# Optimization experiments

Hardware: AMD Instinct MI355X
Metric: run time of the kernel (lower is better)

Reference implementation:

```python
import jax, jax.numpy as jnp
import numpy as np

B, T = 32, 2048            # batch, seq_len
V = 16                     # vocab_size
H = 256                    # hidden_size
NV = V + 2                 # embedding rows (padding_idx=0 + vocab + delimiter)
NO = V + 1                 # head output size


def setup_inputs() -> dict:
    key = jax.random.key(0)
    ks = jax.random.split(key, 8)
    s = 1.0 / np.sqrt(H).astype(np.float32)
    tokens = jax.random.randint(ks[0], (B, T), 0, NV)
    embed = jax.random.normal(ks[1], (NV, H), jnp.float32) * 0.02
    embed = embed.at[0].set(0.0)  # padding_idx=0
    # GRU params (PyTorch layout: gates [r|z|n] stacked on last dim)
    W_ih = jax.random.uniform(ks[2], (H, 3 * H), jnp.float32, -s, s)
    W_hh = jax.random.uniform(ks[3], (H, 3 * H), jnp.float32, -s, s)
    b_ih = jax.random.uniform(ks[4], (3 * H,), jnp.float32, -s, s)
    b_hh = jax.random.uniform(ks[5], (3 * H,), jnp.float32, -s, s)
    W_head = jax.random.uniform(ks[6], (H, NO), jnp.float32, -s, s)
    b_head = jax.random.uniform(ks[7], (NO,), jnp.float32, -s, s)
    return {"tokens": tokens, "embed": embed, "W_ih": W_ih, "W_hh": W_hh,
            "b_ih": b_ih, "b_hh": b_hh, "W_head": W_head, "b_head": b_head}


def _mogru_scan(x, W_ih, W_hh, b_ih, b_hh):
    # x: [B, T, H]. Precompute all input projections in one big GEMM.
    gi = x @ W_ih + b_ih                      # [B, T, 3H]
    gi_t = jnp.swapaxes(gi, 0, 1)             # [T, B, 3H] for scan
    h0 = jnp.zeros((x.shape[0], W_hh.shape[0]), x.dtype)

    def step(h, gi_step):
        gh = h @ W_hh + b_hh                  # [B, 3H]
        i_r, i_z, i_n = jnp.split(gi_step, 3, axis=-1)
        h_r, h_z, h_n = jnp.split(gh, 3, axis=-1)
        r = jax.nn.sigmoid(i_r + h_r)
        z = jax.nn.sigmoid(i_z + h_z)         # beta: retention gate
        n = jnp.tanh(i_n + r * h_n)
        h_new = (1.0 - z) * n + z * h
        return h_new, (h_new, z)

    h_last, (outs, betas) = jax.lax.scan(step, h0, gi_t)
    return jnp.swapaxes(outs, 0, 1), h_last, jnp.swapaxes(betas, 0, 1)


def reference(tokens, embed, W_ih, W_hh, b_ih, b_hh, W_head, b_head):
    x = embed[tokens]                          # [B, T, H] embedding lookup
    output, _, betas = _mogru_scan(x, W_ih, W_hh, b_ih, b_hh)
    logits = output @ W_head + b_head          # [B, T, V+1]
    return logits, betas
```

## Files before the change

### kernel.cpp

```cpp
#include <hip/hip_runtime.h>

#define BB   32
#define TT   2048
#define HH   256
#define G3   768
#define NVOC 18
#define NOUT 17
#define LOGITS_ELEMS ((size_t)BB * TT * NOUT)

typedef _Float16 h2 __attribute__((ext_vector_type(2)));

__device__ __forceinline__ float bf1(unsigned short u){
  union{unsigned int i; float f;} v; v.i = ((unsigned int)u) << 16; return v.f;
}
__device__ __forceinline__ unsigned short f2bf(float f){
  union{float f; unsigned int i;} v; v.f = f;
  unsigned int lsb = (v.i >> 16) & 1u;
  v.i += 0x7fffu + lsb;
  return (unsigned short)(v.i >> 16);
}
__device__ __forceinline__ float bflo(unsigned int u){
  union{unsigned int i; float f;} v; v.i = u << 16; return v.f;
}
__device__ __forceinline__ float bfhi(unsigned int u){
  union{unsigned int i; float f;} v; v.i = u & 0xffff0000u; return v.f;
}

__device__ __forceinline__ float ld1(const float* p, size_t i){ return p[i]; }
__device__ __forceinline__ float ld1(const unsigned short* p, size_t i){ return bf1(p[i]); }

__device__ __forceinline__ bool detect_f32(const void* W_ih_raw){
  const unsigned short* u = (const unsigned short*)W_ih_raw;
  bool big = false;
  #pragma unroll
  for (int i = 0; i < 64; i++){
    float v = bf1(u[i]);
    big |= !(v >= -0.25f && v <= 0.25f);
  }
  return big;
}

#if __has_builtin(__builtin_amdgcn_fdot2)
#define FDOT2(a,b,c) __builtin_amdgcn_fdot2((a),(b),(c),false)
#else
#define FDOT2(a,b,c) ((c) + (float)(a).x*(float)(b).x + (float)(a).y*(float)(b).y)
#endif

template<typename T>
__device__ __forceinline__ void prep_body(const T* W_hh, _Float16* Wp){
  int j = blockIdx.x;
  int e = threadIdx.x;
  int q = j & 1, p = j >> 1;
  int c = e >> 7, i = e & 127;
  float v = ld1(W_hh, (size_t)(128*q + i) * G3 + 2*p + c);
  Wp[(size_t)j * 256 + e] = (_Float16)v;
}

__global__ __launch_bounds__(256) void k_prep(
    const void* __restrict__ W_hh, const void* __restrict__ W_ih,
    _Float16* __restrict__ Wp)
{
  if (detect_f32(W_ih)) prep_body<float>((const float*)W_hh, Wp);
  else                  prep_body<unsigned short>((const unsigned short*)W_hh, Wp);
}

template<typename T>
__device__ __forceinline__ void proj_body(const T* embed, const T* W_ih,
                                          const T* b_ih, const T* b_hh,
                                          float* proj, float* bb){
  __shared__ float s_e[HH];
  int v = blockIdx.x, j = threadIdx.x;
  if (j < HH) s_e[j] = ld1(embed, (size_t)v * HH + j);
  if (v == 0) bb[j] = ld1(b_hh, (size_t)j);
  __syncthreads();
  float acc = ld1(b_ih, (size_t)j);
  #pragma unroll 8
  for (int k = 0; k < HH; k++)
    acc += s_e[k] * ld1(W_ih, (size_t)k * G3 + j);
  proj[(size_t)v * G3 + j] = acc;
}

__global__ __launch_bounds__(768) void k_proj(
    const void* __restrict__ embed, const void* __restrict__ W_ih,
    const void* __restrict__ b_ih, const void* __restrict__ b_hh,
    float* __restrict__ proj, float* __restrict__ bb)
{
  if (detect_f32(W_ih))
    proj_body<float>((const float*)embed, (const float*)W_ih,
                     (const float*)b_ih, (const float*)b_hh, proj, bb);
  else
    proj_body<unsigned short>((const unsigned short*)embed,
                              (const unsigned short*)W_ih,
                              (const unsigned short*)b_ih,
                              (const unsigned short*)b_hh, proj, bb);
}

__global__ __launch_bounds__(768, 1) void k_scan(
    const int*      __restrict__ tokens,
    const _Float16* __restrict__ Wp,
    const float*    __restrict__ bb,
    const void*     __restrict__ W_ih,
    const float*    __restrict__ proj,
    unsigned short* __restrict__ outs,
    void*           __restrict__ d_out_base)
{
  __shared__ float s_proj[NVOC * G3];
  __shared__ __align__(16) h2 s_h[HH / 2];
  __shared__ float s_z[HH];
  __shared__ float s_n[HH];

  const bool f32m = detect_f32(W_ih);
  const int b = blockIdx.x;
  const int j = threadIdx.x;
  const int q16 = (j & 1) * 16;

  for (int i = j; i < NVOC * G3; i += 768) s_proj[i] = proj[i];

  h2 wA[64], wB[64];
  {
    const float4* wp4 = (const float4*)(Wp + (size_t)j * 256);
    #pragma unroll
    for (int i = 0; i < 16; i++){
      float4 v = wp4[i];
      wA[4*i+0] = __builtin_bit_cast(h2, v.x);
      wA[4*i+1] = __builtin_bit_cast(h2, v.y);
      wA[4*i+2] = __builtin_bit_cast(h2, v.z);
      wA[4*i+3] = __builtin_bit_cast(h2, v.w);
    }
    #pragma unroll
    for (int i = 0; i < 16; i++){
      float4 v = wp4[16 + i];
      wB[4*i+0] = __builtin_bit_cast(h2, v.x);
      wB[4*i+1] = __builtin_bit_cast(h2, v.y);
      wB[4*i+2] = __builtin_bit_cast(h2, v.z);
      wB[4*i+3] = __builtin_bit_cast(h2, v.w);
    }
  }
  const float bhh = bb[j];

  if (j < HH/2) { h2 z; z.x = (_Float16)0.f; z.y = (_Float16)0.f; s_h[j] = z; }
  float h_old = 0.f;

  const int* tptr = tokens + (size_t)b * TT;
  int tok = tptr[0];
  unsigned short* orow   = outs + (size_t)b * TT * HH + j;
  unsigned short* brow_b = (unsigned short*)d_out_base + LOGITS_ELEMS
                           + (size_t)b * TT * HH + (j - HH);
  float*          brow_f = (float*)d_out_base + LOGITS_ELEMS
                           + (size_t)b * TT * HH + (j - HH);

  __syncthreads();

  for (int t = 0; t < TT; t++) {
    int tok_next = (t + 1 < TT) ? tptr[t + 1] : 0;
    const float* pj = s_proj + tok * G3;
    float gi  = pj[j];
    float gin = (j < HH) ? pj[2*HH + j] : 0.f;

    float a0 = 0.f, a1 = 0.f, a2 = 0.f, a3 = 0.f;
    const int4* hp = (const int4*)s_h;
    #pragma unroll
    for (int i = 0; i < 16; i++) {
      int4 hv = hp[q16 + i];
      h2 x0 = __builtin_bit_cast(h2, hv.x);
      h2 x1 = __builtin_bit_cast(h2, hv.y);
      h2 x2 = __builtin_bit_cast(h2, hv.z);
      h2 x3 = __builtin_bit_cast(h2, hv.w);
      a0 = FDOT2(wA[4*i+0], x0, a0);
      a1 = FDOT2(wA[4*i+1], x1, a1);
      a0 = FDOT2(wA[4*i+2], x2, a0);
      a1 = FDOT2(wA[4*i+3], x3, a1);
      a2 = FDOT2(wB[4*i+0], x0, a2);
      a3 = FDOT2(wB[4*i+1], x1, a3);
      a2 = FDOT2(wB[4*i+2], x2, a2);
      a3 = FDOT2(wB[4*i+3], x3, a3);
    }
    float accA = a0 + a1;
    float accB = a2 + a3;
    accA += __shfl_xor(accA, 1);
    accB += __shfl_xor(accB, 1);
    float gh = ((j & 1) ? accB : accA) + bhh;

    float r = 0.f;
    if (j >= 2*HH) {
      s_n[j - 2*HH] = gh;
    } else if (j >= HH) {
      float z = 1.f / (1.f + __expf(-(gi + gh)));
      s_z[j - HH] = z;
      if (f32m) brow_f[(size_t)t * HH] = z;
      else      brow_b[(size_t)t * HH] = f2bf(z);
    } else {
      r = 1.f / (1.f + __expf(-(gi + gh)));
    }
    __syncthreads();

    if (j < HH) {
      float z = s_z[j];
      float x = gin + r * s_n[j];
      x = fminf(fmaxf(x, -15.f), 15.f);
      float e = __expf(2.f * x);
      float n = (e - 1.f) / (e + 1.f);
      float hn = (1.f - z) * n + z * h_old;
      h_old = hn;
      ((_Float16*)s_h)[j] = (_Float16)hn;
      orow[(size_t)t * HH] = f2bf(hn);
    }
    __syncthreads();
    tok = tok_next;
  }
}

template<typename T>
__device__ __forceinline__ void stage_head(const T* W_head, const T* b_head,
                                           float* s_w, float* s_b, int tid){
  for (int i = tid; i < NOUT * HH; i += 256) {
    int o = i / HH, k = i - o * HH;
    s_w[i] = ld1(W_head, (size_t)k * NOUT + o);
  }
  if (tid < NOUT) s_b[tid] = ld1(b_head, (size_t)tid);
}

__global__ __launch_bounds__(256) void k_head(
    const unsigned short* __restrict__ outs,
    const void* __restrict__ W_head,
    const void* __restrict__ b_head,
    const void* __restrict__ W_ih,
    void* __restrict__ logits_out)
{
  __shared__ float s_w[NOUT * HH];
  __shared__ float s_b[NOUT];
  const bool f32m = detect_f32(W_ih);
  const int tid = threadIdx.x;

  if (f32m) stage_head<float>((const float*)W_head, (const float*)b_head,
                              s_w, s_b, tid);
  else      stage_head<unsigned short>((const unsigned short*)W_head,
                                       (const unsigned short*)b_head,
                                       s_w, s_b, tid);
  __syncthreads();

  size_t gid = (size_t)blockIdx.x * 256 + tid;
  if (gid >= LOGITS_ELEMS) return;
  int o = (int)(gid % NOUT);
  size_t row = gid / NOUT;

  const uint4* xp = (const uint4*)(outs + row * HH);
  const float* wv = s_w + o * HH;
  float a0 = 0.f, a1 = 0.f, a2 = 0.f, a3 = 0.f;
  #pragma unroll 8
  for (int kk = 0; kk < 32; kk++) {
    uint4 u = xp[kk];
    int kb = kk * 8;
    a0 += bflo(u.x) * wv[kb+0] + bfhi(u.x) * wv[kb+1];
    a1 += bflo(u.y) * wv[kb+2] + bfhi(u.y) * wv[kb+3];
    a2 += bflo(u.z) * wv[kb+4] + bfhi(u.z) * wv[kb+5];
    a3 += bflo(u.w) * wv[kb+6] + bfhi(u.w) * wv[kb+7];
  }
  float val = ((a0 + a1) + (a2 + a3)) + s_b[o];
  if (f32m) ((float*)logits_out)[gid] = val;
  else      ((unsigned short*)logits_out)[gid] = f2bf(val);
}

extern "C" void kernel_launch(void* const* d_in, const int* in_sizes, int n_in,
                              void* d_out, int out_size, void* d_ws, size_t ws_size,
                              hipStream_t stream)
{
  const int* tokens = (const int*)d_in[0];
  const void* embed  = d_in[1];
  const void* W_ih   = d_in[2];
  const void* W_hh   = d_in[3];
  const void* b_ih   = d_in[4];
  const void* b_hh   = d_in[5];
  const void* W_head = d_in[6];
  const void* b_head = d_in[7];

  char* ws = (char*)d_ws;
  float*          proj = (float*)ws;
  float*          bb   = (float*)(ws + 55296);
  _Float16*       Wp   = (_Float16*)(ws + 55296 + 3072);
  unsigned short* outs = (unsigned short*)(ws + 55296 + 3072 + 393216);

  k_prep<<<G3, 256, 0, stream>>>(W_hh, W_ih, Wp);
  k_proj<<<NVOC, G3, 0, stream>>>(embed, W_ih, b_ih, b_hh, proj, bb);
  k_scan<<<BB, G3, 0, stream>>>(tokens, Wp, bb, W_ih, proj, outs, d_out);
  k_head<<<(int)((LOGITS_ELEMS + 255) / 256), 256, 0, stream>>>(
      outs, W_head, b_head, W_ih, d_out);
}
```

Before: 2.718 ms.

## Restructure GRU scan to 512 threads with all three gates per pair and double-buffered h

The scan kernel now uses 512 threads, where each thread pair owns one hidden unit and computes its r, z and n gate dot products from 192 register-resident fp16 weight pairs. The gate combine runs in registers instead of through shared memory. Double-buffering the hidden state cuts the per-step barriers from two to one. The r/z parts of b_hh are folded into the precomputed input projection, the weight prep layout is rewritten to match, and the h buffers are padded to avoid bank conflicts. The cost is much higher register pressure (192 h2 weights per thread), which could cause spills.

Result: slower. 2.786 ms (+2.5%).

```diff
diff --git a/kernel.cpp b/kernel.cpp
--- a/kernel.cpp
+++ b/kernel.cpp
@@ -47,18 +47,24 @@
 #endif
 
 template<typename T>
-__device__ __forceinline__ void prep_body(const T* W_hh, _Float16* Wp){
-  int j = blockIdx.x;
-  int e = threadIdx.x;
-  int q = j & 1, p = j >> 1;
-  int c = e >> 7, i = e & 127;
-  float v = ld1(W_hh, (size_t)(128*q + i) * G3 + 2*p + c);
-  Wp[(size_t)j * 256 + e] = (_Float16)v;
+__device__ __forceinline__ void prep_body(const T* W_hh, unsigned int* Wp){
+  unsigned int e = blockIdx.x * 256 + threadIdx.x;
+  unsigned int c = e & 3, tmp = e >> 2;
+  unsigned int tid = tmp & 511, f = tmp >> 9;
+  unsigned int m = (f << 2) | c;
+  unsigned int g = m >> 6, kk = m & 63;
+  unsigned int u = tid >> 1, q = tid & 1;
+  unsigned int col = g * 256 + u;
+  unsigned int k0 = q * 128 + kk * 2;
+  float lo = ld1(W_hh, (size_t)k0 * G3 + col);
+  float hi = ld1(W_hh, (size_t)(k0 + 1) * G3 + col);
+  h2 t; t.x = (_Float16)lo; t.y = (_Float16)hi;
+  Wp[e] = __builtin_bit_cast(unsigned int, t);
 }
 
 __global__ __launch_bounds__(256) void k_prep(
     const void* __restrict__ W_hh, const void* __restrict__ W_ih,
-    _Float16* __restrict__ Wp)
+    unsigned int* __restrict__ Wp)
 {
   if (detect_f32(W_ih)) prep_body<float>((const float*)W_hh, Wp);
   else                  prep_body<unsigned short>((const unsigned short*)W_hh, Wp);
@@ -74,6 +80,7 @@
   if (v == 0) bb[j] = ld1(b_hh, (size_t)j);
   __syncthreads();
   float acc = ld1(b_ih, (size_t)j);
+  if (j < 2 * HH) acc += ld1(b_hh, (size_t)j);
   #pragma unroll 8
   for (int k = 0; k < HH; k++)
     acc += s_e[k] * ld1(W_ih, (size_t)k * G3 + j);
@@ -95,119 +102,115 @@
                               (const unsigned short*)b_hh, proj, bb);
 }
 
-__global__ __launch_bounds__(768, 1) void k_scan(
-    const int*      __restrict__ tokens,
-    const _Float16* __restrict__ Wp,
-    const float*    __restrict__ bb,
-    const void*     __restrict__ W_ih,
-    const float*    __restrict__ proj,
-    unsigned short* __restrict__ outs,
-    void*           __restrict__ d_out_base)
-{
-  __shared__ float s_proj[NVOC * G3];
-  __shared__ __align__(16) h2 s_h[HH / 2];
-  __shared__ float s_z[HH];
-  __shared__ float s_n[HH];
+#define SPROJ_PAD 6656
+
+__global__ __launch_bounds__(512, 1) void k_scan(
+    const int*          __restrict__ tokens,
+    const unsigned int* __restrict__ Wp,
+    const float*        __restrict__ bb,
+    const void*         __restrict__ W_ih,
+    const float*        __restrict__ proj,
+    unsigned short*     __restrict__ outs,
+    void*               __restrict__ d_out_base)
+{
+  __shared__ float s_proj[NVOC * G3 + SPROJ_PAD];
+  __shared__ __align__(16) unsigned int s_hA[136];
+  __shared__ __align__(16) unsigned int s_hB[136];
 
   const bool f32m = detect_f32(W_ih);
-  const int b = blockIdx.x;
-  const int j = threadIdx.x;
-  const int q16 = (j & 1) * 16;
-
-  for (int i = j; i < NVOC * G3; i += 768) s_proj[i] = proj[i];
-
-  h2 wA[64], wB[64];
+  const int b   = blockIdx.x;
+  const int tid = threadIdx.x;
+  const int u   = tid >> 1;
+  const int q   = tid & 1;
+
+  for (int i = tid; i < NVOC * G3; i += 512) s_proj[i] = proj[i];
+
+  h2 w[192];
   {
-    const float4* wp4 = (const float4*)(Wp + (size_t)j * 256);
+    const float4* wp4 = (const float4*)Wp;
     #pragma unroll
-    for (int i = 0; i < 16; i++){
-      float4 v = wp4[i];
-      wA[4*i+0] = __builtin_bit_cast(h2, v.x);
-      wA[4*i+1] = __builtin_bit_cast(h2, v.y);
-      wA[4*i+2] = __builtin_bit_cast(h2, v.z);
-      wA[4*i+3] = __builtin_bit_cast(h2, v.w);
+    for (int f = 0; f < 48; f++) {
+      float4 v = wp4[(size_t)f * 512 + tid];
+      w[4*f+0] = __builtin_bit_cast(h2, v.x);
+      w[4*f+1] = __builtin_bit_cast(h2, v.y);
+      w[4*f+2] = __builtin_bit_cast(h2, v.z);
+      w[4*f+3] = __builtin_bit_cast(h2, v.w);
     }
-    #pragma unroll
-    for (int i = 0; i < 16; i++){
-      float4 v = wp4[16 + i];
-      wB[4*i+0] = __builtin_bit_cast(h2, v.x);
-      wB[4*i+1] = __builtin_bit_cast(h2, v.y);
-      wB[4*i+2] = __builtin_bit_cast(h2, v.z);
-      wB[4*i+3] = __builtin_bit_cast(h2, v.w);
-    }
-  }
-  const float bhh = bb[j];
-
-  if (j < HH/2) { h2 z; z.x = (_Float16)0.f; z.y = (_Float16)0.f; s_h[j] = z; }
+  }
+  const float bbn = bb[2 * HH + u];
+
+  if (tid < 136) s_hA[tid] = 0u;
   float h_old = 0.f;
 
   const int* tptr = tokens + (size_t)b * TT;
   int tok = tptr[0];
-  unsigned short* orow   = outs + (size_t)b * TT * HH + j;
+  unsigned short* orow   = outs + (size_t)b * TT * HH + u;
   unsigned short* brow_b = (unsigned short*)d_out_base + LOGITS_ELEMS
-                           + (size_t)b * TT * HH + (j - HH);
+                           + (size_t)b * TT * HH + u;
   float*          brow_f = (float*)d_out_base + LOGITS_ELEMS
-                           + (size_t)b * TT * HH + (j - HH);
+                           + (size_t)b * TT * HH + u;
 
   __syncthreads();
 
-  for (int t = 0; t < TT; t++) {
-    int tok_next = (t + 1 < TT) ? tptr[t + 1] : 0;
-    const float* pj = s_proj + tok * G3;
-    float gi  = pj[j];
-    float gin = (j < HH) ? pj[2*HH + j] : 0.f;
-
-    float a0 = 0.f, a1 = 0.f, a2 = 0.f, a3 = 0.f;
-    const int4* hp = (const int4*)s_h;
-    #pragma unroll
-    for (int i = 0; i < 16; i++) {
-      int4 hv = hp[q16 + i];
-      h2 x0 = __builtin_bit_cast(h2, hv.x);
-      h2 x1 = __builtin_bit_cast(h2, hv.y);
-      h2 x2 = __builtin_bit_cast(h2, hv.z);
-      h2 x3 = __builtin_bit_cast(h2, hv.w);
-      a0 = FDOT2(wA[4*i+0], x0, a0);
-      a1 = FDOT2(wA[4*i+1], x1, a1);
-      a0 = FDOT2(wA[4*i+2], x2, a0);
-      a1 = FDOT2(wA[4*i+3], x3, a1);
-      a2 = FDOT2(wB[4*i+0], x0, a2);
-      a3 = FDOT2(wB[4*i+1], x1, a3);
-      a2 = FDOT2(wB[4*i+2], x2, a2);
-      a3 = FDOT2(wB[4*i+3], x3, a3);
-    }
-    float accA = a0 + a1;
-    float accB = a2 + a3;
-    accA += __shfl_xor(accA, 1);
-    accB += __shfl_xor(accB, 1);
-    float gh = ((j & 1) ? accB : accA) + bhh;
-
-    float r = 0.f;
-    if (j >= 2*HH) {
-      s_n[j - 2*HH] = gh;
-    } else if (j >= HH) {
-      float z = 1.f / (1.f + __expf(-(gi + gh)));
-      s_z[j - HH] = z;
-      if (f32m) brow_f[(size_t)t * HH] = z;
-      else      brow_b[(size_t)t * HH] = f2bf(z);
-    } else {
-      r = 1.f / (1.f + __expf(-(gi + gh)));
-    }
-    __syncthreads();
-
-    if (j < HH) {
-      float z = s_z[j];
-      float x = gin + r * s_n[j];
-      x = fminf(fmaxf(x, -15.f), 15.f);
-      float e = __expf(2.f * x);
-      float n = (e - 1.f) / (e + 1.f);
-      float hn = (1.f - z) * n + z * h_old;
-      h_old = hn;
-      ((_Float16*)s_h)[j] = (_Float16)hn;
-      orow[(size_t)t * HH] = f2bf(hn);
-    }
-    __syncthreads();
-    tok = tok_next;
-  }
+#define STEP(T, RB, WB)                                                      \
+  {                                                                          \
+    int tok_cur = tok;                                                       \
+    tok = ((T) + 1 < TT) ? tptr[(T) + 1] : 0;                                \
+    const float* pj = s_proj + tok_cur * G3;                                 \
+    float gir = pj[u], giz = pj[HH + u], gin = pj[2*HH + u];                 \
+    const int4* hp = (const int4*)(RB);                                      \
+    float ar[4] = {0.f,0.f,0.f,0.f};                                         \
+    float az[4] = {0.f,0.f,0.f,0.f};                                         \
+    float an[4] = {0.f,0.f,0.f,0.f};                                         \
+    _Pragma("unroll")                                                        \
+    for (int i = 0; i < 16; i++) {                                           \
+      int4 hv = hp[q * 17 + i];                                              \
+      h2 x0 = __builtin_bit_cast(h2, hv.x);                                  \
+      h2 x1 = __builtin_bit_cast(h2, hv.y);                                  \
+      h2 x2 = __builtin_bit_cast(h2, hv.z);                                  \
+      h2 x3 = __builtin_bit_cast(h2, hv.w);                                  \
+      ar[0] = FDOT2(w[4*i+0],       x0, ar[0]);                              \
+      ar[1] = FDOT2(w[4*i+1],       x1, ar[1]);                              \
+      ar[2] = FDOT2(w[4*i+2],       x2, ar[2]);                              \
+      ar[3] = FDOT2(w[4*i+3],       x3, ar[3]);                              \
+      az[0] = FDOT2(w[64+4*i+0],    x0, az[0]);                              \
+      az[1] = FDOT2(w[64+4*i+1],    x1, az[1]);                              \
+      az[2] = FDOT2(w[64+4*i+2],    x2, az[2]);                              \
+      az[3] = FDOT2(w[64+4*i+3],    x3, az[3]);                              \
+      an[0] = FDOT2(w[128+4*i+0],   x0, an[0]);                              \
+      an[1] = FDOT2(w[128+4*i+1],   x1, an[1]);                              \
+      an[2] = FDOT2(w[128+4*i+2],   x2, an[2]);                              \
+      an[3] = FDOT2(w[128+4*i+3],   x3, an[3]);                              \
+    }                                                                        \
+    float gr = (ar[0] + ar[1]) + (ar[2] + ar[3]);                            \
+    float gz = (az[0] + az[1]) + (az[2] + az[3]);                            \
+    float gn = (an[0] + an[1]) + (an[2] + an[3]);                            \
+    gr += __shfl_xor(gr, 1);                                                 \
+    gz += __shfl_xor(gz, 1);                                                 \
+    gn += __shfl_xor(gn, 1);                                                 \
+    float r = 1.f / (1.f + __expf(-(gir + gr)));                             \
+    float z = 1.f / (1.f + __expf(-(giz + gz)));                             \
+    float x = gin + r * (gn + bbn);                                          \
+    x = fminf(fmaxf(x, -15.f), 15.f);                                        \
+    float ex = __expf(2.f * x);                                              \
+    float n = (ex - 1.f) / (ex + 1.f);                                       \
+    float hn = (1.f - z) * n + z * h_old;                                    \
+    h_old = hn;                                                              \
+    if (q == 0) {                                                            \
+      ((_Float16*)(WB))[(u >> 7) * 136 + (u & 127)] = (_Float16)hn;          \
+      orow[(size_t)(T) * HH] = f2bf(hn);                                     \
+    } else {                                                                 \
+      if (f32m) brow_f[(size_t)(T) * HH] = z;                                \
+      else      brow_b[(size_t)(T) * HH] = f2bf(z);                          \
+    }                                                                        \
+    __syncthreads();                                                         \
+  }
+
+  for (int t = 0; t < TT; t += 2) {
+    STEP(t,     s_hA, s_hB)
+    STEP(t + 1, s_hB, s_hA)
+  }
+#undef STEP
 }
 
 template<typename T>
@@ -277,12 +280,12 @@
   char* ws = (char*)d_ws;
   float*          proj = (float*)ws;
   float*          bb   = (float*)(ws + 55296);
-  _Float16*       Wp   = (_Float16*)(ws + 55296 + 3072);
+  unsigned int*   Wp   = (unsigned int*)(ws + 55296 + 3072);
   unsigned short* outs = (unsigned short*)(ws + 55296 + 3072 + 393216);
 
-  k_prep<<<G3, 256, 0, stream>>>(W_hh, W_ih, Wp);
+  k_prep<<<384, 256, 0, stream>>>(W_hh, W_ih, Wp);
   k_proj<<<NVOC, G3, 0, stream>>>(embed, W_ih, b_ih, b_hh, proj, bb);
-  k_scan<<<BB, G3, 0, stream>>>(tokens, Wp, bb, W_ih, proj, outs, d_out);
+  k_scan<<<BB, 512, 0, stream>>>(tokens, Wp, bb, W_ih, proj, outs, d_out);
   k_head<<<(int)((LOGITS_ELEMS + 255) / 256), 256, 0, stream>>>(
       outs, W_head, b_head, W_ih, d_out);
 }
```
